# Performance work log

Hardware: AMD Instinct MI355X
Metric: run time of the kernel (lower is better)

## Reference

```python
import jax, jax.numpy as jnp
import numpy as np

B, C, W, H, HEADS = 32, 512, 32, 32, 8
D = C // HEADS
N = W * H
LN_EPS = 1e-5


def setup_inputs() -> dict:
    key = jax.random.key(0)
    ks = jax.random.split(key, 11)
    s = 1.0 / np.sqrt(C)
    return {
        "x": jax.random.normal(ks[0], (B, C, W, H), jnp.float32),
        "Wq": jax.random.normal(ks[1], (C, C), jnp.float32) * s,
        "bq": jax.random.normal(ks[2], (C,), jnp.float32) * 0.01,
        "Wk": jax.random.normal(ks[3], (C, C), jnp.float32) * s,
        "bk": jax.random.normal(ks[4], (C,), jnp.float32) * 0.01,
        "Wv": jax.random.normal(ks[5], (C, C), jnp.float32) * s,
        "bv": jax.random.normal(ks[6], (C,), jnp.float32) * 0.01,
        "rel_h": jax.random.normal(ks[7], (1, HEADS, D, 1, H), jnp.float32),
        "rel_w": jax.random.normal(ks[8], (1, HEADS, D, W, 1), jnp.float32),
        "ln_w": jnp.ones((C, W, H), jnp.float32),
        "ln_b": jnp.zeros((C, W, H), jnp.float32),
    }


def reference(x, Wq, bq, Wk, bk, Wv, bv, rel_h, rel_w, ln_w, ln_b):
    b, c, w, h = x.shape
    nh, d, n = HEADS, c // HEADS, w * h

    def proj(Wm, bm):
        # 1x1 conv == per-pixel linear: out[b,o,w,h] = sum_c Wm[o,c] x[b,c,w,h] + bm[o]
        y = jnp.einsum('bcwh,oc->bowh', x, Wm) + bm[None, :, None, None]
        return y.reshape(b, nh, d, n)

    q = proj(Wq, bq)  # [B,h,d,N]
    k = proj(Wk, bk)
    v = proj(Wv, bv)

    # content-content: q^T k -> [B,h,N,N]
    cc = jnp.einsum('bhdn,bhdm->bhnm', q, k)
    # content-position: (rel_h + rel_w) flattened to [h,d,N], permuted, matmul with q
    pos = (rel_h + rel_w).reshape(nh, d, n)  # [h,d,N]
    cp = jnp.einsum('hdn,bhdm->bhnm', pos, q)

    attn = jax.nn.softmax(cc + cp, axis=-1)  # [B,h,N,N]
    # out = v @ attn^T  -> [B,h,d,N]
    out = jnp.einsum('bhdn,bhmn->bhdm', v, attn)
    out = out.reshape(b, c, w, h)

    # LayerNorm over [C,W,H] with elementwise affine, then residual
    mu = jnp.mean(out, axis=(1, 2, 3), keepdims=True)
    var = jnp.var(out, axis=(1, 2, 3), keepdims=True)
    out = (out - mu) * jax.lax.rsqrt(var + LN_EPS) * ln_w[None] + ln_b[None]
    return out + x
```

## Files before the change

### kernel.cpp

```cpp
#include <hip/hip_runtime.h>
#include <stdint.h>

typedef _Float16 f16x8 __attribute__((ext_vector_type(8)));
typedef _Float16 f16x4 __attribute__((ext_vector_type(4)));
typedef float f32x4  __attribute__((ext_vector_type(4)));

__device__ __forceinline__ _Float16 f2h(float f){ return (_Float16)f; }

#define NB   32
#define NC   512
#define NH   8
#define ND   64
#define NN   1024

__global__ __launch_bounds__(256) void wt_conv(const float* __restrict__ Wq,
                                               const float* __restrict__ Wk,
                                               const float* __restrict__ Wv,
                                               _Float16* __restrict__ Wt){
  int idx = blockIdx.x * 256 + threadIdx.x;
  int sel = idx >> 18;
  const float* W = (sel == 0) ? Wq : (sel == 1) ? Wk : Wv;
  Wt[idx] = f2h(W[idx & 262143]);
}

__global__ __launch_bounds__(256) void transpose_x(const float* __restrict__ x,
                                                   _Float16* __restrict__ xT){
  __shared__ float tile[32][33];
  int n0 = blockIdx.x * 32, c0 = blockIdx.y * 32, b = blockIdx.z;
  int t = threadIdx.x;
  int tn = t & 31, tc = t >> 5;
#pragma unroll
  for (int k = 0; k < 4; k++)
    tile[tc + 8*k][tn] = x[(b*NC + c0 + tc + 8*k)*NN + n0 + tn];
  __syncthreads();
#pragma unroll
  for (int k = 0; k < 4; k++)
    xT[(b*NN + n0 + tc + 8*k)*NC + c0 + tn] = f2h(tile[tn][tc + 8*k]);
}

__global__ __launch_bounds__(256) void pos_conv(const float* __restrict__ rel_h,
                                                const float* __restrict__ rel_w,
                                                _Float16* __restrict__ pos_t){
  int idx = blockIdx.x * 256 + threadIdx.x;
  int d = idx & 63, n = (idx >> 6) & 1023, h = idx >> 16;
  int ww = n >> 5, hh = n & 31;
  float v = rel_h[(h*ND + d)*32 + hh] + rel_w[(h*ND + d)*32 + ww];
  pos_t[idx] = f2h(v);
}

#define ASTR 72
#define TSTR 136

__global__ __launch_bounds__(256) void proj_gemm(const _Float16* __restrict__ Wt,
                                                 const _Float16* __restrict__ xT,
                                                 const float* __restrict__ bq,
                                                 const float* __restrict__ bk,
                                                 const float* __restrict__ bv,
                                                 _Float16* __restrict__ q_ws,
                                                 _Float16* __restrict__ k_ws,
                                                 _Float16* __restrict__ v_ws){
  __shared__ _Float16 smem[2 * 128 * ASTR];
  _Float16* As = smem;
  _Float16* Bs = smem + 128 * ASTR;

  int mt = blockIdx.x;
  int nt = blockIdx.y;
  int b  = blockIdx.z;
  int t = threadIdx.x, lane = t & 63, w = t >> 6;
  int wm = w >> 1, wn = w & 1;
  int lr = lane & 15, lg = lane >> 4;

  f32x4 acc[4][4];
#pragma unroll
  for (int i = 0; i < 4; i++)
#pragma unroll
    for (int j = 0; j < 4; j++) acc[i][j] = (f32x4)0.f;

  const _Float16* Arow = Wt + mt * 128 * NC;
  const _Float16* Brow = xT + (b * NN + nt * 128) * NC;

  for (int k0 = 0; k0 < NC; k0 += 64){
    __syncthreads();
#pragma unroll
    for (int i = 0; i < 4; i++){
      int lin = t + 256 * i;
      int row = lin >> 3, c8 = lin & 7;
      *(f16x8*)(As + row*ASTR + c8*8) = *(const f16x8*)(Arow + row*NC + k0 + c8*8);
      *(f16x8*)(Bs + row*ASTR + c8*8) = *(const f16x8*)(Brow + row*NC + k0 + c8*8);
    }
    __syncthreads();
#pragma unroll
    for (int ks = 0; ks < 2; ks++){
      f16x8 af[4], bfr[4];
#pragma unroll
      for (int mi = 0; mi < 4; mi++)
        af[mi] = *(f16x8*)(As + (wm*64 + mi*16 + lr)*ASTR + ks*32 + lg*8);
#pragma unroll
      for (int nj = 0; nj < 4; nj++)
        bfr[nj] = *(f16x8*)(Bs + (wn*64 + nj*16 + lr)*ASTR + ks*32 + lg*8);
#pragma unroll
      for (int mi = 0; mi < 4; mi++)
#pragma unroll
        for (int nj = 0; nj < 4; nj++)
          acc[mi][nj] = __builtin_amdgcn_mfma_f32_16x16x32_f16(af[mi], bfr[nj], acc[mi][nj], 0, 0, 0);
    }
  }
  __syncthreads();

  if (mt < 8){
    _Float16* Ts = smem;
#pragma unroll
    for (int mi = 0; mi < 4; mi++){
      int o0 = wm*64 + mi*16 + 4*lg;
      int og = mt*128 + o0;
      int sel = og >> 9, oo = og & 511;
      const float* bias = (sel == 0) ? bq : bk;
      float b0 = bias[oo], b1 = bias[oo+1], b2 = bias[oo+2], b3 = bias[oo+3];
#pragma unroll
      for (int nj = 0; nj < 4; nj++){
        int pix = wn*64 + nj*16 + lr;
        f16x4 pk;
        pk[0] = f2h(acc[mi][nj][0] + b0);
        pk[1] = f2h(acc[mi][nj][1] + b1);
        pk[2] = f2h(acc[mi][nj][2] + b2);
        pk[3] = f2h(acc[mi][nj][3] + b3);
        *(f16x4*)(Ts + pix*TSTR + o0) = pk;
      }
    }
    __syncthreads();
#pragma unroll
    for (int i = 0; i < 8; i++){
      int lin = t + 256 * i;
      int c_o = lin & 15, pix = lin >> 4;
      f16x8 v = *(f16x8*)(Ts + pix*TSTR + c_o*8);
      int og = mt*128 + c_o*8;
      int sel = og >> 9, oo = og & 511;
      int head = oo >> 6, d = oo & 63;
      _Float16* dst = (sel == 0) ? q_ws : k_ws;
      *(f16x8*)(dst + (((b*NH + head)*NN) + nt*128 + pix)*ND + d) = v;
    }
  } else {
    _Float16* Ts2 = smem;
#pragma unroll
    for (int mi = 0; mi < 4; mi++){
      int o0 = wm*64 + mi*16 + 4*lg;
      int vb = (mt - 8)*128 + o0;
      float b0 = bv[vb], b1 = bv[vb+1], b2 = bv[vb+2], b3 = bv[vb+3];
#pragma unroll
      for (int nj = 0; nj < 4; nj++){
        int pix = wn*64 + nj*16 + lr;
        Ts2[(o0+0)*TSTR + pix] = f2h(acc[mi][nj][0] + b0);
        Ts2[(o0+1)*TSTR + pix] = f2h(acc[mi][nj][1] + b1);
        Ts2[(o0+2)*TSTR + pix] = f2h(acc[mi][nj][2] + b2);
        Ts2[(o0+3)*TSTR + pix] = f2h(acc[mi][nj][3] + b3);
      }
    }
    __syncthreads();
#pragma unroll
    for (int i = 0; i < 8; i++){
      int lin = t + 256 * i;
      int pix8 = lin & 15, o_loc = lin >> 4;
      f16x8 v = *(f16x8*)(Ts2 + o_loc*TSTR + pix8*8);
      int vb = (mt - 8)*128 + o_loc;
      int head = vb >> 6, d = vb & 63;
      *(f16x8*)(v_ws + ((b*NH + head)*ND + d)*NN + nt*128 + pix8*8) = v;
    }
  }
}

#define KSTR 136
#define VSTR 72
#define PSTR 72
#define OSTR 65
#define OFF_VT 8704
#define OFF_P  13312

__global__ __launch_bounds__(256, 3) void attn_kernel(const _Float16* __restrict__ q_ws,
                                                      const _Float16* __restrict__ k_ws,
                                                      const _Float16* __restrict__ v_ws,
                                                      const _Float16* __restrict__ pos_t,
                                                      float* __restrict__ out){
  __shared__ _Float16 smem[22528];
  _Float16* Kc = smem;
  _Float16* Vt = smem + OFF_VT;
  _Float16* Pl = smem + OFF_P;

  int bid = blockIdx.x;
  int sid = (bid & 7) * 256 + (bid >> 3);
  int qt = sid & 7, h = (sid >> 3) & 7, b = sid >> 6;

  int t = threadIdx.x, lane = t & 63, w = t >> 6;
  int lr = lane & 15, lg = lane >> 4;

  const _Float16* qbh = q_ws + (b*NH + h) * NN * ND;
  const _Float16* kbh = k_ws + (b*NH + h) * NN * ND;
  const _Float16* vbh = v_ws + (b*NH + h) * ND * NN;
  const _Float16* pph = pos_t + h * NN * ND;

  f16x8 qreg[2][4];
#pragma unroll
  for (int qi = 0; qi < 2; qi++){
    int row = qt*128 + w*32 + qi*16 + lr;
#pragma unroll
    for (int ks = 0; ks < 4; ks++){
      const _Float16* src = (ks < 2) ? (qbh + row*ND + ks*32 + lg*8)
                                     : (pph + row*ND + (ks-2)*32 + lg*8);
      qreg[qi][ks] = *(const f16x8*)src;
    }
  }

  float m_r[2], l_r[2];
  f32x4 oacc[2][4];
#pragma unroll
  for (int qi = 0; qi < 2; qi++){ m_r[qi] = -1e30f; l_r[qi] = 0.f; }
#pragma unroll
  for (int qi = 0; qi < 2; qi++)
#pragma unroll
    for (int dj = 0; dj < 4; dj++) oacc[qi][dj] = (f32x4)0.f;

  for (int n0 = 0; n0 < NN; n0 += 64){
    __syncthreads();
#pragma unroll
    for (int i = 0; i < 4; i++){
      int lin = t + 256*i;
      int row = lin >> 4, c8 = lin & 15;
      const _Float16* src = (c8 < 8) ? (kbh + (n0 + row)*ND + c8*8)
                                     : (qbh + (n0 + row)*ND + (c8 - 8)*8);
      *(f16x8*)(Kc + row*KSTR + c8*8) = *(const f16x8*)src;
    }
#pragma unroll
    for (int i = 0; i < 2; i++){
      int lin = t + 256*i;
      int d = lin >> 3, ch = lin & 7;
      *(f16x8*)(Vt + d*VSTR + ch*8) = *(const f16x8*)(vbh + d*NN + n0 + ch*8);
    }
    __syncthreads();

    f32x4 sacc[4][2];
#pragma unroll
    for (int kt = 0; kt < 4; kt++)
#pragma unroll
      for (int qi = 0; qi < 2; qi++) sacc[kt][qi] = (f32x4)0.f;
#pragma unroll
    for (int ks = 0; ks < 4; ks++){
      f16x8 kf[4];
#pragma unroll
      for (int kt = 0; kt < 4; kt++)
        kf[kt] = *(f16x8*)(Kc + (kt*16 + lr)*KSTR + ks*32 + lg*8);
#pragma unroll
      for (int kt = 0; kt < 4; kt++)
#pragma unroll
        for (int qi = 0; qi < 2; qi++)
          sacc[kt][qi] = __builtin_amdgcn_mfma_f32_16x16x32_f16(kf[kt], qreg[qi][ks], sacc[kt][qi], 0, 0, 0);
    }

#pragma unroll
    for (int qi = 0; qi < 2; qi++){
      float mx = sacc[0][qi][0];
#pragma unroll
      for (int kt = 0; kt < 4; kt++)
#pragma unroll
        for (int r = 0; r < 4; r++) mx = fmaxf(mx, sacc[kt][qi][r]);
      mx = fmaxf(mx, __shfl_xor(mx, 16));
      mx = fmaxf(mx, __shfl_xor(mx, 32));
      float mn = fmaxf(m_r[qi], mx);
      float cr = __expf(m_r[qi] - mn);
      m_r[qi] = mn;
      float ts = 0.f;
#pragma unroll
      for (int kt = 0; kt < 4; kt++){
        float p0 = __expf(sacc[kt][qi][0] - mn);
        float p1 = __expf(sacc[kt][qi][1] - mn);
        float p2 = __expf(sacc[kt][qi][2] - mn);
        float p3 = __expf(sacc[kt][qi][3] - mn);
        ts += (p0 + p1) + (p2 + p3);
        f16x4 pk;
        pk[0] = f2h(p0); pk[1] = f2h(p1); pk[2] = f2h(p2); pk[3] = f2h(p3);
        *(f16x4*)(Pl + (w*32 + qi*16 + lr)*PSTR + kt*16 + lg*4) = pk;
      }
      ts += __shfl_xor(ts, 16);
      ts += __shfl_xor(ts, 32);
      l_r[qi] = l_r[qi]*cr + ts;
#pragma unroll
      for (int r = 0; r < 4; r++){
        float crow = __shfl(cr, 4*lg + r);
#pragma unroll
        for (int dj = 0; dj < 4; dj++) oacc[qi][dj][r] *= crow;
      }
    }

#pragma unroll
    for (int ks = 0; ks < 2; ks++){
      f16x8 pf[2], vf[4];
#pragma unroll
      for (int qi = 0; qi < 2; qi++)
        pf[qi] = *(f16x8*)(Pl + (w*32 + qi*16 + lr)*PSTR + ks*32 + lg*8);
#pragma unroll
      for (int dj = 0; dj < 4; dj++)
        vf[dj] = *(f16x8*)(Vt + (dj*16 + lr)*VSTR + ks*32 + lg*8);
#pragma unroll
      for (int qi = 0; qi < 2; qi++)
#pragma unroll
        for (int dj = 0; dj < 4; dj++)
          oacc[qi][dj] = __builtin_amdgcn_mfma_f32_16x16x32_f16(pf[qi], vf[dj], oacc[qi][dj], 0, 0, 0);
    }
  }

  __syncthreads();
  float* Ot = (float*)smem;
#pragma unroll
  for (int qi = 0; qi < 2; qi++){
    float iv = 1.f / l_r[qi];
#pragma unroll
    for (int r = 0; r < 4; r++){
      float invr = __shfl(iv, 4*lg + r);
#pragma unroll
      for (int dj = 0; dj < 4; dj++)
        Ot[(w*32 + qi*16 + 4*lg + r)*OSTR + dj*16 + lr] = oacc[qi][dj][r] * invr;
    }
  }
  __syncthreads();

#pragma unroll
  for (int i = 0; i < 8; i++){
    int lin = t + 256*i;
    int jc = lin & 31, d = lin >> 5;
    float4 v;
    v.x = Ot[(jc*4 + 0)*OSTR + d];
    v.y = Ot[(jc*4 + 1)*OSTR + d];
    v.z = Ot[(jc*4 + 2)*OSTR + d];
    v.w = Ot[(jc*4 + 3)*OSTR + d];
    *(float4*)(out + (b*NC + h*ND + d)*NN + qt*128 + jc*4) = v;
  }
}

__global__ __launch_bounds__(256) void ln_partial(const float* __restrict__ out,
                                                  float* __restrict__ red){
  int i = blockIdx.x, b = blockIdx.y, t = threadIdx.x;
  const float4* p = (const float4*)(out + b*524288 + i*65536);
  float s = 0.f, sq = 0.f;
  for (int k = t; k < 16384; k += 256){
    float4 v = p[k];
    s  += v.x + v.y + v.z + v.w;
    sq += v.x*v.x + v.y*v.y + v.z*v.z + v.w*v.w;
  }
  for (int off = 32; off; off >>= 1){ s += __shfl_down(s, off); sq += __shfl_down(sq, off); }
  __shared__ float ls[8];
  int w = t >> 6, lane = t & 63;
  if (lane == 0){ ls[w*2] = s; ls[w*2 + 1] = sq; }
  __syncthreads();
  if (t == 0){
    red[(b*8 + i)*2]     = ls[0] + ls[2] + ls[4] + ls[6];
    red[(b*8 + i)*2 + 1] = ls[1] + ls[3] + ls[5] + ls[7];
  }
}

__global__ void ln_stats(const float* __restrict__ red, float* __restrict__ stats){
  int b = threadIdx.x;
  if (b < 32){
    float s = 0.f, sq = 0.f;
    for (int j = 0; j < 8; j++){ s += red[(b*8 + j)*2]; sq += red[(b*8 + j)*2 + 1]; }
    float mu  = s * (1.f / 524288.f);
    float var = sq * (1.f / 524288.f) - mu*mu;
    stats[b*2] = mu;
    stats[b*2 + 1] = rsqrtf(var + 1e-5f);
  }
}

__global__ __launch_bounds__(256) void ln_apply(const float* __restrict__ x,
                                                const float* __restrict__ lw,
                                                const float* __restrict__ lb,
                                                const float* __restrict__ stats,
                                                float* __restrict__ out){
  int tid = blockIdx.x*256 + threadIdx.x;
  for (int i4 = tid; i4 < 4194304; i4 += 524288){
    int b = i4 >> 17;
    int r4 = i4 & 131071;
    float mu = stats[b*2], rs = stats[b*2 + 1];
    float4 o  = ((const float4*)out)[i4];
    float4 xv = ((const float4*)x)[i4];
    float4 ww = ((const float4*)lw)[r4];
    float4 bb = ((const float4*)lb)[r4];
    o.x = (o.x - mu)*rs*ww.x + bb.x + xv.x;
    o.y = (o.y - mu)*rs*ww.y + bb.y + xv.y;
    o.z = (o.z - mu)*rs*ww.z + bb.z + xv.z;
    o.w = (o.w - mu)*rs*ww.w + bb.w + xv.w;
    ((float4*)out)[i4] = o;
  }
}

extern "C" void kernel_launch(void* const* d_in, const int* in_sizes, int n_in,
                              void* d_out, int out_size, void* d_ws, size_t ws_size,
                              hipStream_t stream){
  (void)in_sizes; (void)n_in; (void)out_size; (void)ws_size;
  const float* x    = (const float*)d_in[0];
  const float* Wq   = (const float*)d_in[1];
  const float* bq   = (const float*)d_in[2];
  const float* Wk   = (const float*)d_in[3];
  const float* bk   = (const float*)d_in[4];
  const float* Wv   = (const float*)d_in[5];
  const float* bv   = (const float*)d_in[6];
  const float* relh = (const float*)d_in[7];
  const float* relw = (const float*)d_in[8];
  const float* lnw  = (const float*)d_in[9];
  const float* lnb  = (const float*)d_in[10];
  float* out = (float*)d_out;
  char* ws = (char*)d_ws;

  _Float16* q_ws  = (_Float16*)(ws);
  _Float16* k_ws  = (_Float16*)(ws + 33554432);
  _Float16* v_ws  = (_Float16*)(ws + 67108864);
  _Float16* xT    = (_Float16*)(ws + 100663296);
  _Float16* Wt    = (_Float16*)(ws + 134217728);
  _Float16* pos_t = (_Float16*)(ws + 135790592);
  float* red   = (float*)(ws + 136839168);
  float* stats = red + 512;

  wt_conv    <<<3072, 256, 0, stream>>>(Wq, Wk, Wv, Wt);
  transpose_x<<<dim3(32, 16, 32), 256, 0, stream>>>(x, xT);
  pos_conv   <<<2048, 256, 0, stream>>>(relh, relw, pos_t);
  proj_gemm  <<<dim3(12, 8, 32), 256, 0, stream>>>(Wt, xT, bq, bk, bv, q_ws, k_ws, v_ws);
  attn_kernel<<<2048, 256, 0, stream>>>(q_ws, k_ws, v_ws, pos_t, out);
  ln_partial <<<dim3(8, 32), 256, 0, stream>>>(out, red);
  ln_stats   <<<1, 64, 0, stream>>>(red, stats);
  ln_apply   <<<2048, 256, 0, stream>>>(x, lnw, lnb, stats, out);
}
```

Before: 319.5 us.

## Fuse LN partial stats into attention, shrink LDS, lazy softmax rescale

Folds the LayerNorm partial sum and sum-of-squares into the attention epilogue and removes the separate ln_partial kernel, so the attention output is not read back a second time. Shared memory is cut by aliasing the P tile onto the K/Q tile (with an extra barrier) and storing V with an XOR swizzle instead of padding. The epilogue is split into two halves so the smaller buffer fits, and launch bounds are raised to allow more resident blocks. Softmax now rescales only when the running max grows by more than 8, and probabilities are packed with cvt_pkrtz. This trades an extra barrier and round-toward-zero fp16 conversion for lower memory traffic and higher occupancy.

Measured after the change: 862.8 us. +170.0%, slower.

```diff
diff --git a/kernel.cpp b/kernel.cpp
--- a/kernel.cpp
+++ b/kernel.cpp
@@ -3,6 +3,7 @@
 
 typedef _Float16 f16x8 __attribute__((ext_vector_type(8)));
 typedef _Float16 f16x4 __attribute__((ext_vector_type(4)));
+typedef __fp16   fp16x2 __attribute__((ext_vector_type(2)));
 typedef float f32x4  __attribute__((ext_vector_type(4)));
 
 __device__ __forceinline__ _Float16 f2h(float f){ return (_Float16)f; }
@@ -169,21 +170,21 @@
 }
 
 #define KSTR 136
-#define VSTR 72
 #define PSTR 72
 #define OSTR 65
-#define OFF_VT 8704
-#define OFF_P  13312
-
-__global__ __launch_bounds__(256, 3) void attn_kernel(const _Float16* __restrict__ q_ws,
+#define OFF_VT 9216
+
+__global__ __launch_bounds__(256, 6) void attn_kernel(const _Float16* __restrict__ q_ws,
                                                       const _Float16* __restrict__ k_ws,
                                                       const _Float16* __restrict__ v_ws,
                                                       const _Float16* __restrict__ pos_t,
-                                                      float* __restrict__ out){
-  __shared__ _Float16 smem[22528];
+                                                      float* __restrict__ out,
+                                                      float* __restrict__ red){
+  __shared__ _Float16 smem[13312];
+  __shared__ float lnred[8];
   _Float16* Kc = smem;
+  _Float16* Pl = smem;
   _Float16* Vt = smem + OFF_VT;
-  _Float16* Pl = smem + OFF_P;
 
   int bid = blockIdx.x;
   int sid = (bid & 7) * 256 + (bid >> 3);
@@ -232,7 +233,7 @@
     for (int i = 0; i < 2; i++){
       int lin = t + 256*i;
       int d = lin >> 3, ch = lin & 7;
-      *(f16x8*)(Vt + d*VSTR + ch*8) = *(const f16x8*)(vbh + d*NN + n0 + ch*8);
+      *(f16x8*)(Vt + d*64 + ((ch*8) ^ ((d & 7) << 3))) = *(const f16x8*)(vbh + d*NN + n0 + ch*8);
     }
     __syncthreads();
 
@@ -254,18 +255,30 @@
           sacc[kt][qi] = __builtin_amdgcn_mfma_f32_16x16x32_f16(kf[kt], qreg[qi][ks], sacc[kt][qi], 0, 0, 0);
     }
 
+    __syncthreads();
+
 #pragma unroll
     for (int qi = 0; qi < 2; qi++){
-      float mx = sacc[0][qi][0];
-#pragma unroll
-      for (int kt = 0; kt < 4; kt++)
-#pragma unroll
-        for (int r = 0; r < 4; r++) mx = fmaxf(mx, sacc[kt][qi][r]);
+      float m0 = fmaxf(fmaxf(sacc[0][qi][0], sacc[0][qi][1]), fmaxf(sacc[0][qi][2], sacc[0][qi][3]));
+      float m1 = fmaxf(fmaxf(sacc[1][qi][0], sacc[1][qi][1]), fmaxf(sacc[1][qi][2], sacc[1][qi][3]));
+      float m2 = fmaxf(fmaxf(sacc[2][qi][0], sacc[2][qi][1]), fmaxf(sacc[2][qi][2], sacc[2][qi][3]));
+      float m3 = fmaxf(fmaxf(sacc[3][qi][0], sacc[3][qi][1]), fmaxf(sacc[3][qi][2], sacc[3][qi][3]));
+      float mx = fmaxf(fmaxf(m0, m1), fmaxf(m2, m3));
       mx = fmaxf(mx, __shfl_xor(mx, 16));
       mx = fmaxf(mx, __shfl_xor(mx, 32));
-      float mn = fmaxf(m_r[qi], mx);
-      float cr = __expf(m_r[qi] - mn);
-      m_r[qi] = mn;
+      if (!__all(mx - m_r[qi] <= 8.f)){
+        float mn = fmaxf(m_r[qi], mx);
+        float cr = __expf(m_r[qi] - mn);
+        m_r[qi] = mn;
+        l_r[qi] *= cr;
+#pragma unroll
+        for (int r = 0; r < 4; r++){
+          float crow = __shfl(cr, 4*lg + r);
+#pragma unroll
+          for (int dj = 0; dj < 4; dj++) oacc[qi][dj][r] *= crow;
+        }
+      }
+      float mn = m_r[qi];
       float ts = 0.f;
 #pragma unroll
       for (int kt = 0; kt < 4; kt++){
@@ -274,19 +287,14 @@
         float p2 = __expf(sacc[kt][qi][2] - mn);
         float p3 = __expf(sacc[kt][qi][3] - mn);
         ts += (p0 + p1) + (p2 + p3);
-        f16x4 pk;
-        pk[0] = f2h(p0); pk[1] = f2h(p1); pk[2] = f2h(p2); pk[3] = f2h(p3);
-        *(f16x4*)(Pl + (w*32 + qi*16 + lr)*PSTR + kt*16 + lg*4) = pk;
+        union { fp16x2 h2[2]; uint2 u2; } pu;
+        pu.h2[0] = __builtin_amdgcn_cvt_pkrtz(p0, p1);
+        pu.h2[1] = __builtin_amdgcn_cvt_pkrtz(p2, p3);
+        *(uint2*)(Pl + (w*32 + qi*16 + lr)*PSTR + kt*16 + lg*4) = pu.u2;
       }
       ts += __shfl_xor(ts, 16);
       ts += __shfl_xor(ts, 32);
-      l_r[qi] = l_r[qi]*cr + ts;
-#pragma unroll
-      for (int r = 0; r < 4; r++){
-        float crow = __shfl(cr, 4*lg + r);
-#pragma unroll
-        for (int dj = 0; dj < 4; dj++) oacc[qi][dj][r] *= crow;
-      }
+      l_r[qi] += ts;
     }
 
 #pragma unroll
@@ -296,8 +304,10 @@
       for (int qi = 0; qi < 2; qi++)
         pf[qi] = *(f16x8*)(Pl + (w*32 + qi*16 + lr)*PSTR + ks*32 + lg*8);
 #pragma unroll
-      for (int dj = 0; dj < 4; dj++)
-        vf[dj] = *(f16x8*)(Vt + (dj*16 + lr)*VSTR + ks*32 + lg*8);
+      for (int dj = 0; dj < 4; dj++){
+        int row = dj*16 + lr;
+        vf[dj] = *(f16x8*)(Vt + row*64 + ((ks*32 + lg*8) ^ ((row & 7) << 3)));
+      }
 #pragma unroll
       for (int qi = 0; qi < 2; qi++)
 #pragma unroll
@@ -306,52 +316,54 @@
     }
   }
 
+  float s_ln = 0.f, q_ln = 0.f;
   __syncthreads();
   float* Ot = (float*)smem;
 #pragma unroll
-  for (int qi = 0; qi < 2; qi++){
-    float iv = 1.f / l_r[qi];
-#pragma unroll
-    for (int r = 0; r < 4; r++){
-      float invr = __shfl(iv, 4*lg + r);
-#pragma unroll
-      for (int dj = 0; dj < 4; dj++)
-        Ot[(w*32 + qi*16 + 4*lg + r)*OSTR + dj*16 + lr] = oacc[qi][dj][r] * invr;
-    }
-  }
-  __syncthreads();
-
-#pragma unroll
-  for (int i = 0; i < 8; i++){
-    int lin = t + 256*i;
-    int jc = lin & 31, d = lin >> 5;
-    float4 v;
-    v.x = Ot[(jc*4 + 0)*OSTR + d];
-    v.y = Ot[(jc*4 + 1)*OSTR + d];
-    v.z = Ot[(jc*4 + 2)*OSTR + d];
-    v.w = Ot[(jc*4 + 3)*OSTR + d];
-    *(float4*)(out + (b*NC + h*ND + d)*NN + qt*128 + jc*4) = v;
-  }
-}
-
-__global__ __launch_bounds__(256) void ln_partial(const float* __restrict__ out,
-                                                  float* __restrict__ red){
-  int i = blockIdx.x, b = blockIdx.y, t = threadIdx.x;
-  const float4* p = (const float4*)(out + b*524288 + i*65536);
-  float s = 0.f, sq = 0.f;
-  for (int k = t; k < 16384; k += 256){
-    float4 v = p[k];
-    s  += v.x + v.y + v.z + v.w;
-    sq += v.x*v.x + v.y*v.y + v.z*v.z + v.w*v.w;
-  }
-  for (int off = 32; off; off >>= 1){ s += __shfl_down(s, off); sq += __shfl_down(sq, off); }
-  __shared__ float ls[8];
-  int w = t >> 6, lane = t & 63;
-  if (lane == 0){ ls[w*2] = s; ls[w*2 + 1] = sq; }
+  for (int p = 0; p < 2; p++){
+    if ((w >> 1) == p){
+      int wl = w & 1;
+#pragma unroll
+      for (int qi = 0; qi < 2; qi++){
+        float iv = 1.f / l_r[qi];
+#pragma unroll
+        for (int r = 0; r < 4; r++){
+          float invr = __shfl(iv, 4*lg + r);
+#pragma unroll
+          for (int dj = 0; dj < 4; dj++){
+            float val = oacc[qi][dj][r] * invr;
+            s_ln += val; q_ln += val*val;
+            Ot[(wl*32 + qi*16 + 4*lg + r)*OSTR + dj*16 + lr] = val;
+          }
+        }
+      }
+    }
+    __syncthreads();
+#pragma unroll
+    for (int i = 0; i < 4; i++){
+      int lin = t + 256*i;
+      int d = lin >> 4, jc = lin & 15;
+      float4 v;
+      v.x = Ot[(jc*4 + 0)*OSTR + d];
+      v.y = Ot[(jc*4 + 1)*OSTR + d];
+      v.z = Ot[(jc*4 + 2)*OSTR + d];
+      v.w = Ot[(jc*4 + 3)*OSTR + d];
+      *(float4*)(out + (b*NC + h*ND + d)*NN + qt*128 + p*64 + jc*4) = v;
+    }
+    __syncthreads();
+  }
+
+#pragma unroll
+  for (int off = 1; off < 64; off <<= 1){
+    s_ln += __shfl_xor(s_ln, off);
+    q_ln += __shfl_xor(q_ln, off);
+  }
+  if (lane == 0){ lnred[w*2] = s_ln; lnred[w*2 + 1] = q_ln; }
   __syncthreads();
   if (t == 0){
-    red[(b*8 + i)*2]     = ls[0] + ls[2] + ls[4] + ls[6];
-    red[(b*8 + i)*2 + 1] = ls[1] + ls[3] + ls[5] + ls[7];
+    int idx = ((b*NH + h)*8 + qt)*2;
+    red[idx]     = lnred[0] + lnred[2] + lnred[4] + lnred[6];
+    red[idx + 1] = lnred[1] + lnred[3] + lnred[5] + lnred[7];
   }
 }
 
@@ -359,7 +371,7 @@
   int b = threadIdx.x;
   if (b < 32){
     float s = 0.f, sq = 0.f;
-    for (int j = 0; j < 8; j++){ s += red[(b*8 + j)*2]; sq += red[(b*8 + j)*2 + 1]; }
+    for (int j = 0; j < 64; j++){ s += red[(b*64 + j)*2]; sq += red[(b*64 + j)*2 + 1]; }
     float mu  = s * (1.f / 524288.f);
     float var = sq * (1.f / 524288.f) - mu*mu;
     stats[b*2] = mu;
@@ -414,14 +426,13 @@
   _Float16* Wt    = (_Float16*)(ws + 134217728);
   _Float16* pos_t = (_Float16*)(ws + 135790592);
   float* red   = (float*)(ws + 136839168);
-  float* stats = red + 512;
+  float* stats = red + 4096;
 
   wt_conv    <<<3072, 256, 0, stream>>>(Wq, Wk, Wv, Wt);
   transpose_x<<<dim3(32, 16, 32), 256, 0, stream>>>(x, xT);
   pos_conv   <<<2048, 256, 0, stream>>>(relh, relw, pos_t);
   proj_gemm  <<<dim3(12, 8, 32), 256, 0, stream>>>(Wt, xT, bq, bk, bv, q_ws, k_ws, v_ws);
-  attn_kernel<<<2048, 256, 0, stream>>>(q_ws, k_ws, v_ws, pos_t, out);
-  ln_partial <<<dim3(8, 32), 256, 0, stream>>>(out, red);
+  attn_kernel<<<2048, 256, 0, stream>>>(q_ws, k_ws, v_ws, pos_t, out, red);
   ln_stats   <<<1, 64, 0, stream>>>(red, stats);
   ln_apply   <<<2048, 256, 0, stream>>>(x, lnw, lnb, stats, out);
 }
```
